# Kernel tuning notes

Measured on AMD Instinct MI355X. Metric: run time of the kernel, lower is better.

## Reference

```python
import jax, jax.numpy as jnp
import numpy as np

CONTRASTIVE_NUM = 2


def setup_inputs() -> dict:
    key = jax.random.key(0)
    k1, k2 = jax.random.split(key)
    N, V = 8192, 32000
    logits = jax.random.normal(k1, (N, V), dtype=jnp.float32)
    target = jax.random.randint(k2, (N,), 0, V, dtype=jnp.int64)
    return {"logits": logits, "target": target}


def reference(logits, target):
    # log_softmax over the class (vocab) dim
    logp = jax.nn.log_softmax(logits, axis=1)              # [N, V]
    # top-k log-probs (torch uses full argsort; only values matter for the sum)
    topk_lp, _ = jax.lax.top_k(logp, CONTRASTIVE_NUM)      # [N, k]
    # gathered target log-prob, kept as [N, 1] to mirror torch broadcasting:
    # (-[N,1] + [N,k]).sum() == sum_i (k * -logp_tgt_i + sum_j topk_ij)
    tgt_lp = jnp.take_along_axis(logp, target[:, None], axis=1)  # [N, 1]
    loss = jnp.sum(-tgt_lp + topk_lp)
    return loss
```

## Files before the change

kernel.cpp:

```cpp
#include <hip/hip_runtime.h>


#define NROWS 8192
#define VOCAB 32000

__device__ __forceinline__ void top2_merge(float& m1, float& m2, float o1, float o2) {
    float nm1 = fmaxf(m1, o1);
    float nm2 = fmaxf(fminf(m1, o1), fmaxf(m2, o2));
    m1 = nm1; m2 = nm2;
}

__global__ __launch_bounds__(256) void cce_row_kernel(const float* __restrict__ logits,
                                                      const int* __restrict__ target,
                                                      float* __restrict__ row_partial) {
    const int row = blockIdx.x;
    const float4* rp = reinterpret_cast<const float4*>(logits + (size_t)row * VOCAB);

    float m1 = -INFINITY, m2 = -INFINITY;
    for (int i = threadIdx.x; i < VOCAB / 4; i += 256) {
        float4 v = rp[i];
        m2 = fmaxf(m2, fminf(m1, v.x)); m1 = fmaxf(m1, v.x);
        m2 = fmaxf(m2, fminf(m1, v.y)); m1 = fmaxf(m1, v.y);
        m2 = fmaxf(m2, fminf(m1, v.z)); m1 = fmaxf(m1, v.z);
        m2 = fmaxf(m2, fminf(m1, v.w)); m1 = fmaxf(m1, v.w);
    }

    #pragma unroll
    for (int off = 32; off > 0; off >>= 1) {
        float o1 = __shfl_xor(m1, off, 64);
        float o2 = __shfl_xor(m2, off, 64);
        top2_merge(m1, m2, o1, o2);
    }

    __shared__ float s1[4], s2[4];
    const int wave = threadIdx.x >> 6;
    const int lane = threadIdx.x & 63;
    if (lane == 0) { s1[wave] = m1; s2[wave] = m2; }
    __syncthreads();

    if (threadIdx.x == 0) {
        m1 = s1[0]; m2 = s2[0];
        #pragma unroll
        for (int w = 1; w < 4; ++w) top2_merge(m1, m2, s1[w], s2[w]);
        const int t = target[row];
        const float tv = logits[(size_t)row * VOCAB + (size_t)t];
        row_partial[row] = m1 + m2 - 2.0f * tv;
    }
}

__global__ __launch_bounds__(256) void cce_reduce_kernel(const float* __restrict__ row_partial,
                                                         float* __restrict__ out) {
    float s = 0.0f;
    for (int i = threadIdx.x; i < NROWS; i += 256) s += row_partial[i];
    #pragma unroll
    for (int off = 32; off > 0; off >>= 1) s += __shfl_xor(s, off, 64);

    __shared__ float ws[4];
    const int wave = threadIdx.x >> 6;
    const int lane = threadIdx.x & 63;
    if (lane == 0) ws[wave] = s;
    __syncthreads();
    if (threadIdx.x == 0) out[0] = ws[0] + ws[1] + ws[2] + ws[3];
}

extern "C" void kernel_launch(void* const* d_in, const int* in_sizes, int n_in,
                              void* d_out, int out_size, void* d_ws, size_t ws_size,
                              hipStream_t stream) {
    const float* logits = (const float*)d_in[0];
    const int* target = (const int*)d_in[1];
    float* out = (float*)d_out;
    float* row_partial = (float*)d_ws;

    cce_row_kernel<<<NROWS, 256, 0, stream>>>(logits, target, row_partial);
    cce_reduce_kernel<<<1, 256, 0, stream>>>(row_partial, out);
}
```

Measured before the change: 191.3 us.

## Assign one wave per row and fuse final reduction via atomics

```diff
diff --git a/kernel.cpp b/kernel.cpp
--- a/kernel.cpp
+++ b/kernel.cpp
@@ -3,22 +3,29 @@
 
 #define NROWS 8192
 #define VOCAB 32000
+#define ROWS_PER_BLOCK 4
 
-__device__ __forceinline__ void top2_merge(float& m1, float& m2, float o1, float o2) {
-    float nm1 = fmaxf(m1, o1);
-    float nm2 = fmaxf(fminf(m1, o1), fmaxf(m2, o2));
-    m1 = nm1; m2 = nm2;
-}
+typedef float floatx4 __attribute__((ext_vector_type(4)));
 
-__global__ __launch_bounds__(256) void cce_row_kernel(const float* __restrict__ logits,
-                                                      const int* __restrict__ target,
-                                                      float* __restrict__ row_partial) {
-    const int row = blockIdx.x;
-    const float4* rp = reinterpret_cast<const float4*>(logits + (size_t)row * VOCAB);
+__global__ __launch_bounds__(256) void cce_kernel(const float* __restrict__ logits,
+                                                  const int* __restrict__ target,
+                                                  float* __restrict__ out) {
+    const int wave = threadIdx.x >> 6;
+    const int lane = threadIdx.x & 63;
+    const int row  = blockIdx.x * ROWS_PER_BLOCK + wave;
+
+    const floatx4* rp = reinterpret_cast<const floatx4*>(logits + (size_t)row * VOCAB);
+
+    float tv = 0.0f;
+    if (lane == 0) {
+        const int t = target[row];
+        tv = logits[(size_t)row * VOCAB + (size_t)t];
+    }
 
     float m1 = -INFINITY, m2 = -INFINITY;
-    for (int i = threadIdx.x; i < VOCAB / 4; i += 256) {
-        float4 v = rp[i];
+    #pragma unroll 5
+    for (int i = lane; i < VOCAB / 4; i += 64) {
+        floatx4 v = __builtin_nontemporal_load(&rp[i]);
         m2 = fmaxf(m2, fminf(m1, v.x)); m1 = fmaxf(m1, v.x);
         m2 = fmaxf(m2, fminf(m1, v.y)); m1 = fmaxf(m1, v.y);
         m2 = fmaxf(m2, fminf(m1, v.z)); m1 = fmaxf(m1, v.z);
@@ -29,38 +36,14 @@
     for (int off = 32; off > 0; off >>= 1) {
         float o1 = __shfl_xor(m1, off, 64);
         float o2 = __shfl_xor(m2, off, 64);
-        top2_merge(m1, m2, o1, o2);
+        float nm1 = fmaxf(m1, o1);
+        float nm2 = fmaxf(fminf(m1, o1), fmaxf(m2, o2));
+        m1 = nm1; m2 = nm2;
     }
 
-    __shared__ float s1[4], s2[4];
-    const int wave = threadIdx.x >> 6;
-    const int lane = threadIdx.x & 63;
-    if (lane == 0) { s1[wave] = m1; s2[wave] = m2; }
-    __syncthreads();
-
-    if (threadIdx.x == 0) {
-        m1 = s1[0]; m2 = s2[0];
-        #pragma unroll
-        for (int w = 1; w < 4; ++w) top2_merge(m1, m2, s1[w], s2[w]);
-        const int t = target[row];
-        const float tv = logits[(size_t)row * VOCAB + (size_t)t];
-        row_partial[row] = m1 + m2 - 2.0f * tv;
+    if (lane == 0) {
+        atomicAdd(out, m1 + m2 - 2.0f * tv);
     }
-}
-
-__global__ __launch_bounds__(256) void cce_reduce_kernel(const float* __restrict__ row_partial,
-                                                         float* __restrict__ out) {
-    float s = 0.0f;
-    for (int i = threadIdx.x; i < NROWS; i += 256) s += row_partial[i];
-    #pragma unroll
-    for (int off = 32; off > 0; off >>= 1) s += __shfl_xor(s, off, 64);
-
-    __shared__ float ws[4];
-    const int wave = threadIdx.x >> 6;
-    const int lane = threadIdx.x & 63;
-    if (lane == 0) ws[wave] = s;
-    __syncthreads();
-    if (threadIdx.x == 0) out[0] = ws[0] + ws[1] + ws[2] + ws[3];
 }
 
 extern "C" void kernel_launch(void* const* d_in, const int* in_sizes, int n_in,
@@ -69,8 +52,7 @@
     const float* logits = (const float*)d_in[0];
     const int* target = (const int*)d_in[1];
     float* out = (float*)d_out;
-    float* row_partial = (float*)d_ws;
 
-    cce_row_kernel<<<NROWS, 256, 0, stream>>>(logits, target, row_partial);
-    cce_reduce_kernel<<<1, 256, 0, stream>>>(row_partial, out);
+    hipMemsetAsync(out, 0, sizeof(float), stream);
+    cce_kernel<<<NROWS / ROWS_PER_BLOCK, 256, 0, stream>>>(logits, target, out);
 }
```

Result: slower. 201.9 us (+5.6%).
